# Kernel optimization log

Measured on AMD Instinct MI355X. Metric: run time of the kernel, lower is better.

Reference implementation:

```python
import jax, jax.numpy as jnp
import numpy as np
from math import factorial, sqrt

LMAX = 5
TAUS = [16, 16, 16, 16, 16, 16]
BATCH = 256


def _cg(j1, m1, j2, m2, j, m):
    """Standard (complex SO(3) basis) Clebsch-Gordan coefficient <j1 m1 j2 m2 | j m>."""
    if m1 + m2 != m or j < abs(j1 - j2) or j > j1 + j2:
        return 0.0
    f = factorial
    pref = sqrt((2 * j + 1) * f(j + j1 - j2) * f(j - j1 + j2) * f(j1 + j2 - j) / f(j1 + j2 + j + 1))
    pref *= sqrt(f(j + m) * f(j - m) * f(j1 - m1) * f(j1 + m1) * f(j2 - m2) * f(j2 + m2))
    kmin = max(0, j2 - j - m1, j1 + m2 - j)
    kmax = min(j1 + j2 - j, j1 - m1, j2 + m2)
    s = 0.0
    for k in range(kmin, kmax + 1):
        s += (-1) ** k / (f(k) * f(j1 + j2 - j - k) * f(j1 - m1 - k) * f(j2 + m2 - k)
                          * f(j - j2 + m1 + k) * f(j - j1 - m2 + k))
    return pref * s


def _pairs():
    # default CGNet ltuples: for each output l, all (l1, l2) with l1 <= l2 and triangle ineq.
    out = []
    for l in range(LMAX + 1):
        for l1 in range(LMAX + 1):
            for l2 in range(l1, LMAX + 1):
                if abs(l1 - l2) <= l <= l1 + l2:
                    out.append((l, l1, l2))
    return out


PAIRS = _pairs()  # 69 (l, l1, l2) tuples for lmax=5


def _cg_mat(l, l1, l2):
    M = np.zeros((2 * l1 + 1, 2 * l2 + 1, 2 * l + 1), dtype=np.float32)
    for m1 in range(-l1, l1 + 1):
        for m2 in range(-l2, l2 + 1):
            m = m1 + m2
            if -l <= m <= l:
                M[m1 + l1, m2 + l2, m + l] = _cg(l1, m1, l2, m2, l, m)
    return M


CG_MATS = {p: _cg_mat(*p) for p in PAIRS}
CUM_TAUS = np.concatenate([[0], (np.asarray(TAUS) * (2 * np.arange(LMAX + 1) + 1)).cumsum()]).astype(int)


def setup_inputs() -> dict:
    key = jax.random.key(0)
    Fs = jax.random.normal(key, (BATCH, int(CUM_TAUS[-1]), 2), dtype=jnp.float32)
    return {"Fs": Fs}


def reference(Fs) -> jnp.ndarray:
    """Sparse CG tensor product: for each (l,l1,l2) combine fragments F_l1, F_l2
    with CG coefficients into the l-output fragment; concat all fragments.
    Output: (B, cumu_tm_FF[-1], 2) with (m, tau) flattening per l fragment."""
    B = Fs.shape[0]
    frR, frI = [], []
    for l in range(LMAX + 1):
        seg = Fs[:, CUM_TAUS[l]:CUM_TAUS[l + 1]].reshape(B, 2 * l + 1, TAUS[l], 2)
        frR.append(seg[..., 0])
        frI.append(seg[..., 1])
    outs = [[] for _ in range(LMAX + 1)]
    for (l, l1, l2) in PAIRS:
        cg = jnp.asarray(CG_MATS[(l, l1, l2)])  # (2l1+1, 2l2+1, 2l+1)
        r1, i1, r2, i2 = frR[l1], frI[l1], frR[l2], frI[l2]
        e = lambda a, b: jnp.einsum('xym,bxi,byj->bmij', cg, a, b)
        oR = e(r1, r2) - e(i1, i2)           # complex multiply, real part
        oI = e(r1, i2) + e(i1, r2)           # imag part
        # (B, 2l+1, tau1*tau2, 2)
        outs[l].append(jnp.stack([oR, oI], axis=-1).reshape(B, 2 * l + 1, -1, 2))
    # per-l: concat channel blocks (t_offsets order), flatten (m, tau), concat over l
    return jnp.concatenate(
        [jnp.concatenate(outs[l], axis=2).reshape(B, -1, 2) for l in range(LMAX + 1)], axis=1)
```

## Files before the change

### kernel.cpp

```cpp
#include <hip/hip_runtime.h>
#include <vector>
#include <cmath>
#include <cstdint>


#define LMAXV 5
#define NTAU 16

static const int CUMT[7] = {0, 16, 64, 144, 256, 400, 576};

constexpr int F_ROWS   = 576;
constexpr int F4_ROWS  = 288;
constexpr int NBATCH   = 256;
constexpr int F4_PER_B = 457 * 128;
constexpr int BLK      = 256;
constexpr int NCHUNK   = 8;
constexpr int NCOEF    = 2211;
constexpr int MAXJC    = 58;

typedef float f32x4 __attribute__((ext_vector_type(4)));


static double factd(int n) { double r = 1.0; for (int i = 2; i <= n; ++i) r *= (double)i; return r; }

static double cg_coef(int j1, int m1, int j2, int m2, int j, int m) {
    if (m1 + m2 != m) return 0.0;
    double pref = std::sqrt((2.0 * j + 1.0) * factd(j + j1 - j2) * factd(j - j1 + j2) *
                            factd(j1 + j2 - j) / factd(j1 + j2 + j + 1));
    pref *= std::sqrt(factd(j + m) * factd(j - m) * factd(j1 - m1) * factd(j1 + m1) *
                      factd(j2 - m2) * factd(j2 + m2));
    int kmin = std::max(0, std::max(j2 - j - m1, j1 + m2 - j));
    int kmax = std::min(j1 + j2 - j, std::min(j1 - m1, j2 + m2));
    double s = 0.0;
    for (int k = kmin; k <= kmax; ++k) {
        s += ((k & 1) ? -1.0 : 1.0) /
             (factd(k) * factd(j1 + j2 - j - k) * factd(j1 - m1 - k) * factd(j2 + m2 - k) *
              factd(j - j2 + m1 + k) * factd(j - j1 - m2 + k));
    }
    return pref * s;
}

struct Tables { std::vector<int4> jobs; std::vector<float> coeffs; };

static const Tables& get_tables() {
    static Tables t = []() {
        Tables t;
        for (int l = 0; l <= LMAXV; ++l) {
            for (int m_idx = 0; m_idx < 2 * l + 1; ++m_idx) {
                int m = m_idx - l;
                for (int l1 = 0; l1 <= LMAXV; ++l1) {
                    for (int l2 = l1; l2 <= LMAXV; ++l2) {
                        if (!(std::abs(l1 - l2) <= l && l <= l1 + l2)) continue;
                        int lo = std::max(-l1, m - l2), hi = std::min(l1, m + l2);
                        int4 jb;
                        jb.x = (CUMT[l1] / 2 + (lo + l1) * 8) * 16;
                        jb.y = (CUMT[l2] / 2 + (m - lo + l2) * 8) * 16;
                        jb.z = hi - lo + 1;
                        jb.w = (int)t.coeffs.size();
                        for (int m1 = lo; m1 <= hi; ++m1)
                            t.coeffs.push_back((float)cg_coef(l1, m1, l2, m - m1, l, m));
                        t.jobs.push_back(jb);
                    }
                }
            }
        }
        return t;
    }();
    return t;
}


#define KBODY(N)                                                              \
    {                                                                         \
        f32x4 a[N], v[N]; float cc[N];                                        \
        _Pragma("unroll")                                                     \
        for (int k = 0; k < N; ++k) {                                         \
            a[k]  = *(const f32x4*)(sFb + ax + k * 128);                      \
            v[k]  = *(const f32x4*)(sFb + vy - k * 128);                      \
            cc[k] = sC[coff + k];                                             \
        }                                                                     \
        _Pragma("unroll")                                                     \
        for (int k = 0; k < N; ++k) {                                         \
            r00 = fmaf(cc[k], a[k].x * v[k].x - a[k].y * v[k].y, r00);        \
            i00 = fmaf(cc[k], a[k].x * v[k].y + a[k].y * v[k].x, i00);        \
            r01 = fmaf(cc[k], a[k].x * v[k].z - a[k].y * v[k].w, r01);        \
            i01 = fmaf(cc[k], a[k].x * v[k].w + a[k].y * v[k].z, i01);        \
            r10 = fmaf(cc[k], a[k].z * v[k].x - a[k].w * v[k].y, r10);        \
            i10 = fmaf(cc[k], a[k].z * v[k].y + a[k].w * v[k].x, i10);        \
            r11 = fmaf(cc[k], a[k].z * v[k].z - a[k].w * v[k].w, r11);        \
            i11 = fmaf(cc[k], a[k].z * v[k].w + a[k].w * v[k].z, i11);        \
        }                                                                     \
    }

__global__ __launch_bounds__(256) void cg_tp_kernel(
    const f32x4* __restrict__ Fs, f32x4* __restrict__ out,
    const int4* __restrict__ jobs, const float* __restrict__ coeffs)
{
    __shared__ f32x4 sF[F4_ROWS];
    __shared__ float sC[NCOEF];
    __shared__ int4  sJ[MAXJC];

    const int tid   = threadIdx.x;
    const int batch = blockIdx.x >> 3;
    const int chunk = blockIdx.x & (NCHUNK - 1);
    const int jbase = chunk * 57;
    const int jcnt  = (chunk == NCHUNK - 1) ? 58 : 57;

    {
        const f32x4* __restrict__ Fb4 = Fs + (size_t)batch * F4_ROWS;
        for (int t = tid; t < F4_ROWS; t += BLK) sF[t] = Fb4[t];
        for (int t = tid; t < NCOEF;   t += BLK) sC[t] = coeffs[t];
        for (int t = tid; t < jcnt;    t += BLK) sJ[t] = jobs[jbase + t];
    }
    __syncthreads();

    const int wv   = tid >> 6;
    const int lane = tid & 63;
    const int ip   = lane >> 3;
    const int jp   = lane & 7;
    const char* __restrict__ sFb = (const char*)sF;

    f32x4* __restrict__ outb =
        out + (size_t)batch * F4_PER_B + (size_t)jbase * 128;

    for (int jj = wv; jj < jcnt; jj += 4) {
        const int4 jbv = sJ[jj];
        const int ax   = __builtin_amdgcn_readfirstlane(jbv.x) + ip * 16;
        const int vy   = __builtin_amdgcn_readfirstlane(jbv.y) + jp * 16;
        const int cnt  = __builtin_amdgcn_readfirstlane(jbv.z);
        const int coff = __builtin_amdgcn_readfirstlane(jbv.w);

        float r00 = 0.f, i00 = 0.f, r01 = 0.f, i01 = 0.f;
        float r10 = 0.f, i10 = 0.f, r11 = 0.f, i11 = 0.f;

        switch (cnt) {
            case 1:  KBODY(1)  break;
            case 2:  KBODY(2)  break;
            case 3:  KBODY(3)  break;
            case 4:  KBODY(4)  break;
            case 5:  KBODY(5)  break;
            case 6:  KBODY(6)  break;
            case 7:  KBODY(7)  break;
            case 8:  KBODY(8)  break;
            case 9:  KBODY(9)  break;
            case 10: KBODY(10) break;
            default: KBODY(11) break;
        }

        f32x4 s0; s0.x = r00; s0.y = i00; s0.z = r01; s0.w = i01;
        f32x4 s1; s1.x = r10; s1.y = i10; s1.z = r11; s1.w = i11;
        f32x4* __restrict__ po = outb + (size_t)jj * 128 + ip * 16 + jp;
        po[0] = s0;
        po[8] = s1;
    }
}


extern "C" void kernel_launch(void* const* d_in, const int* in_sizes, int n_in,
                              void* d_out, int out_size, void* d_ws, size_t ws_size,
                              hipStream_t stream) {
    const Tables& t = get_tables();

    char*  ws       = (char*)d_ws;
    int4*  d_jobs   = (int4*)ws;
    size_t jbytes   = t.jobs.size() * sizeof(int4);
    size_t coff     = (jbytes + 255) & ~(size_t)255;
    float* d_coeffs = (float*)(ws + coff);

    hipMemcpyAsync(d_jobs, t.jobs.data(), jbytes, hipMemcpyHostToDevice, stream);
    hipMemcpyAsync(d_coeffs, t.coeffs.data(), t.coeffs.size() * sizeof(float),
                   hipMemcpyHostToDevice, stream);

    const f32x4* Fs  = (const f32x4*)d_in[0];
    f32x4*       out = (f32x4*)d_out;

    cg_tp_kernel<<<NBATCH * NCHUNK, BLK, 0, stream>>>(Fs, out, d_jobs, d_coeffs);
}
```

Before: 57.57 us.

## Make blocks persistent over batches with work-balanced job groups and double-buffered inputs

Blocks now iterate over 32 batches each instead of one. The 457 jobs are split into 128 groups balanced by coefficient count, and each block loads the coefficient and job tables once into LDS. The next batch's fragment is prefetched into registers while the current batch is computed, then written to the other LDS buffer. This amortises the table loads and balances work across blocks, at the cost of fewer blocks (1024), a barrier per phase, and more LDS per block.

```diff
diff --git a/kernel.cpp b/kernel.cpp
--- a/kernel.cpp
+++ b/kernel.cpp
@@ -9,14 +9,15 @@
 
 static const int CUMT[7] = {0, 16, 64, 144, 256, 400, 576};
 
-constexpr int F_ROWS   = 576;
 constexpr int F4_ROWS  = 288;
+constexpr int FBYTES   = F4_ROWS * 16;
 constexpr int NBATCH   = 256;
 constexpr int F4_PER_B = 457 * 128;
 constexpr int BLK      = 256;
-constexpr int NCHUNK   = 8;
+constexpr int NJOBS    = 457;
 constexpr int NCOEF    = 2211;
-constexpr int MAXJC    = 58;
+constexpr int NGRP     = 128;
+constexpr int NPHASE   = 32;
 
 typedef float f32x4 __attribute__((ext_vector_type(4)));
 
@@ -40,7 +41,7 @@
     return pref * s;
 }
 
-struct Tables { std::vector<int4> jobs; std::vector<float> coeffs; };
+struct Tables { std::vector<int4> jobs; std::vector<float> coeffs; std::vector<uint16_t> grp; };
 
 static const Tables& get_tables() {
     static Tables t = []() {
@@ -64,6 +65,15 @@
                 }
             }
         }
+        t.grp.assign(NGRP + 1, 0);
+        int total = 0; for (auto& j : t.jobs) total += j.z;
+        int jpos = 0; long cum = 0;
+        for (int g = 0; g < NGRP; ++g) {
+            t.grp[g] = (uint16_t)jpos;
+            long target = ((long)total * (g + 1) + NGRP / 2) / NGRP;
+            while (jpos < NJOBS && cum < target) { cum += t.jobs[jpos].z; ++jpos; }
+        }
+        t.grp[NGRP] = (uint16_t)NJOBS;
         return t;
     }();
     return t;
@@ -92,66 +102,84 @@
         }                                                                     \
     }
 
-__global__ __launch_bounds__(256) void cg_tp_kernel(
+__global__ __launch_bounds__(256, 4) void cg_tp_kernel(
     const f32x4* __restrict__ Fs, f32x4* __restrict__ out,
-    const int4* __restrict__ jobs, const float* __restrict__ coeffs)
+    const int4* __restrict__ jobs, const float* __restrict__ coeffs,
+    const uint16_t* __restrict__ grp)
 {
-    __shared__ f32x4 sF[F4_ROWS];
+    __shared__ f32x4 sF[2][F4_ROWS];
     __shared__ float sC[NCOEF];
-    __shared__ int4  sJ[MAXJC];
+    __shared__ int4  sJ[NJOBS];
 
     const int tid   = threadIdx.x;
-    const int batch = blockIdx.x >> 3;
-    const int chunk = blockIdx.x & (NCHUNK - 1);
-    const int jbase = chunk * 57;
-    const int jcnt  = (chunk == NCHUNK - 1) ? 58 : 57;
-
+    const int gid   = blockIdx.x & (NGRP - 1);
+    const int blane = blockIdx.x >> 7;
+
+    for (int t = tid; t < NCOEF; t += BLK) sC[t] = coeffs[t];
+    for (int t = tid; t < NJOBS; t += BLK) sJ[t] = jobs[t];
     {
-        const f32x4* __restrict__ Fb4 = Fs + (size_t)batch * F4_ROWS;
-        for (int t = tid; t < F4_ROWS; t += BLK) sF[t] = Fb4[t];
-        for (int t = tid; t < NCOEF;   t += BLK) sC[t] = coeffs[t];
-        for (int t = tid; t < jcnt;    t += BLK) sJ[t] = jobs[jbase + t];
+        const f32x4* __restrict__ F0 = Fs + (size_t)blane * F4_ROWS;
+        sF[0][tid] = F0[tid];
+        if (tid < F4_ROWS - BLK) sF[0][BLK + tid] = F0[BLK + tid];
     }
     __syncthreads();
+
+    const int js = grp[gid], je = grp[gid + 1];
 
     const int wv   = tid >> 6;
     const int lane = tid & 63;
     const int ip   = lane >> 3;
     const int jp   = lane & 7;
-    const char* __restrict__ sFb = (const char*)sF;
-
-    f32x4* __restrict__ outb =
-        out + (size_t)batch * F4_PER_B + (size_t)jbase * 128;
-
-    for (int jj = wv; jj < jcnt; jj += 4) {
-        const int4 jbv = sJ[jj];
-        const int ax   = __builtin_amdgcn_readfirstlane(jbv.x) + ip * 16;
-        const int vy   = __builtin_amdgcn_readfirstlane(jbv.y) + jp * 16;
-        const int cnt  = __builtin_amdgcn_readfirstlane(jbv.z);
-        const int coff = __builtin_amdgcn_readfirstlane(jbv.w);
-
-        float r00 = 0.f, i00 = 0.f, r01 = 0.f, i01 = 0.f;
-        float r10 = 0.f, i10 = 0.f, r11 = 0.f, i11 = 0.f;
-
-        switch (cnt) {
-            case 1:  KBODY(1)  break;
-            case 2:  KBODY(2)  break;
-            case 3:  KBODY(3)  break;
-            case 4:  KBODY(4)  break;
-            case 5:  KBODY(5)  break;
-            case 6:  KBODY(6)  break;
-            case 7:  KBODY(7)  break;
-            case 8:  KBODY(8)  break;
-            case 9:  KBODY(9)  break;
-            case 10: KBODY(10) break;
-            default: KBODY(11) break;
-        }
-
-        f32x4 s0; s0.x = r00; s0.y = i00; s0.z = r01; s0.w = i01;
-        f32x4 s1; s1.x = r10; s1.y = i10; s1.z = r11; s1.w = i11;
-        f32x4* __restrict__ po = outb + (size_t)jj * 128 + ip * 16 + jp;
-        po[0] = s0;
-        po[8] = s1;
+
+    for (int p = 0; p < NPHASE; ++p) {
+        const int batch = p * 8 + blane;
+
+        f32x4 r0, r1;
+        if (p < NPHASE - 1) {
+            const f32x4* __restrict__ Fn = Fs + (size_t)(batch + 8) * F4_ROWS;
+            r0 = Fn[tid];
+            if (tid < F4_ROWS - BLK) r1 = Fn[BLK + tid];
+        }
+
+        const char* __restrict__ sFb = (const char*)&sF[p & 1][0];
+        f32x4* __restrict__ outb = out + (size_t)batch * F4_PER_B;
+
+        for (int jj = js + wv; jj < je; jj += 4) {
+            const int4 jbv = sJ[jj];
+            const int ax   = __builtin_amdgcn_readfirstlane(jbv.x) + ip * 16;
+            const int vy   = __builtin_amdgcn_readfirstlane(jbv.y) + jp * 16;
+            const int cnt  = __builtin_amdgcn_readfirstlane(jbv.z);
+            const int coff = __builtin_amdgcn_readfirstlane(jbv.w);
+
+            float r00 = 0.f, i00 = 0.f, r01 = 0.f, i01 = 0.f;
+            float r10 = 0.f, i10 = 0.f, r11 = 0.f, i11 = 0.f;
+
+            switch (cnt) {
+                case 1:  KBODY(1)  break;
+                case 2:  KBODY(2)  break;
+                case 3:  KBODY(3)  break;
+                case 4:  KBODY(4)  break;
+                case 5:  KBODY(5)  break;
+                case 6:  KBODY(6)  break;
+                case 7:  KBODY(7)  break;
+                case 8:  KBODY(8)  break;
+                case 9:  KBODY(9)  break;
+                case 10: KBODY(10) break;
+                default: KBODY(11) break;
+            }
+
+            f32x4 s0; s0.x = r00; s0.y = i00; s0.z = r01; s0.w = i01;
+            f32x4 s1; s1.x = r10; s1.y = i10; s1.z = r11; s1.w = i11;
+            f32x4* __restrict__ po = outb + (size_t)jj * 128 + ip * 16 + jp;
+            po[0] = s0;
+            po[8] = s1;
+        }
+
+        if (p < NPHASE - 1) {
+            sF[(p + 1) & 1][tid] = r0;
+            if (tid < F4_ROWS - BLK) sF[(p + 1) & 1][BLK + tid] = r1;
+        }
+        __syncthreads();
     }
 }
 
@@ -161,18 +189,22 @@
                               hipStream_t stream) {
     const Tables& t = get_tables();
 
-    char*  ws       = (char*)d_ws;
-    int4*  d_jobs   = (int4*)ws;
-    size_t jbytes   = t.jobs.size() * sizeof(int4);
-    size_t coff     = (jbytes + 255) & ~(size_t)255;
-    float* d_coeffs = (float*)(ws + coff);
-
-    hipMemcpyAsync(d_jobs, t.jobs.data(), jbytes, hipMemcpyHostToDevice, stream);
+    char*     ws       = (char*)d_ws;
+    int4*     d_jobs   = (int4*)ws;
+    size_t    coff     = (NJOBS * sizeof(int4) + 255) & ~(size_t)255;
+    float*    d_coeffs = (float*)(ws + coff);
+    size_t    goff     = (coff + NCOEF * sizeof(float) + 255) & ~(size_t)255;
+    uint16_t* d_grp    = (uint16_t*)(ws + goff);
+
+    hipMemcpyAsync(d_jobs, t.jobs.data(), t.jobs.size() * sizeof(int4),
+                   hipMemcpyHostToDevice, stream);
     hipMemcpyAsync(d_coeffs, t.coeffs.data(), t.coeffs.size() * sizeof(float),
                    hipMemcpyHostToDevice, stream);
+    hipMemcpyAsync(d_grp, t.grp.data(), t.grp.size() * sizeof(uint16_t),
+                   hipMemcpyHostToDevice, stream);
 
     const f32x4* Fs  = (const f32x4*)d_in[0];
     f32x4*       out = (f32x4*)d_out;
 
-    cg_tp_kernel<<<NBATCH * NCHUNK, BLK, 0, stream>>>(Fs, out, d_jobs, d_coeffs);
-}
+    cg_tp_kernel<<<NGRP * 8, BLK, 0, stream>>>(Fs, out, d_jobs, d_coeffs, d_grp);
+}
```

Result: slower. 86.48 us (+50.2%).

## Split work per batch into two cost-balanced halves with 512-thread blocks

Applied to the files above, without the earlier changes.

Replaces eight fixed job chunks of 256 threads per batch with two 512-thread blocks per batch, split at the point where the cumulative coefficient count reaches half. This cuts the redundant loading of inputs and the coefficient table into shared memory from eight times to twice per batch, and balances the work between the two blocks. The per-count switch over fully unrolled bodies is replaced by a loop unrolled by four plus a small remainder switch, which shrinks code size but may lengthen dependency chains. Fewer, larger blocks (512 total) may leave some compute units underused.

```diff
diff --git a/kernel.cpp b/kernel.cpp
--- a/kernel.cpp
+++ b/kernel.cpp
@@ -9,14 +9,12 @@
 
 static const int CUMT[7] = {0, 16, 64, 144, 256, 400, 576};
 
-constexpr int F_ROWS   = 576;
 constexpr int F4_ROWS  = 288;
 constexpr int NBATCH   = 256;
 constexpr int F4_PER_B = 457 * 128;
-constexpr int BLK      = 256;
-constexpr int NCHUNK   = 8;
+constexpr int BLK      = 512;
+constexpr int NJOBS    = 457;
 constexpr int NCOEF    = 2211;
-constexpr int MAXJC    = 58;
 
 typedef float f32x4 __attribute__((ext_vector_type(4)));
 
@@ -40,7 +38,7 @@
     return pref * s;
 }
 
-struct Tables { std::vector<int4> jobs; std::vector<float> coeffs; };
+struct Tables { std::vector<int4> jobs; std::vector<float> coeffs; int split; };
 
 static const Tables& get_tables() {
     static Tables t = []() {
@@ -64,20 +62,24 @@
                 }
             }
         }
+        int total = 0; for (auto& j : t.jobs) total += j.z;
+        int cum = 0, s = 0;
+        for (int j = 0; j < NJOBS; ++j) { cum += t.jobs[j].z; if (cum * 2 >= total) { s = j + 1; break; } }
+        t.split = s;
         return t;
     }();
     return t;
 }
 
 
-#define KBODY(N)                                                              \
+#define QBODY(N)                                                              \
     {                                                                         \
         f32x4 a[N], v[N]; float cc[N];                                        \
         _Pragma("unroll")                                                     \
         for (int k = 0; k < N; ++k) {                                         \
-            a[k]  = *(const f32x4*)(sFb + ax + k * 128);                      \
-            v[k]  = *(const f32x4*)(sFb + vy - k * 128);                      \
-            cc[k] = sC[coff + k];                                             \
+            a[k]  = *(const f32x4*)(sFb + axq + k * 128);                     \
+            v[k]  = *(const f32x4*)(sFb + vyq - k * 128);                     \
+            cc[k] = sC[coq + k];                                              \
         }                                                                     \
         _Pragma("unroll")                                                     \
         for (int k = 0; k < N; ++k) {                                         \
@@ -92,27 +94,29 @@
         }                                                                     \
     }
 
-__global__ __launch_bounds__(256) void cg_tp_kernel(
+__global__ __launch_bounds__(512, 4) void cg_tp_kernel(
     const f32x4* __restrict__ Fs, f32x4* __restrict__ out,
-    const int4* __restrict__ jobs, const float* __restrict__ coeffs)
+    const int4* __restrict__ jobs, const float* __restrict__ coeffs,
+    int split)
 {
     __shared__ f32x4 sF[F4_ROWS];
     __shared__ float sC[NCOEF];
-    __shared__ int4  sJ[MAXJC];
+    __shared__ int4  sJ[NJOBS];
 
     const int tid   = threadIdx.x;
-    const int batch = blockIdx.x >> 3;
-    const int chunk = blockIdx.x & (NCHUNK - 1);
-    const int jbase = chunk * 57;
-    const int jcnt  = (chunk == NCHUNK - 1) ? 58 : 57;
+    const int batch = blockIdx.x >> 1;
+    const int chunk = blockIdx.x & 1;
 
     {
         const f32x4* __restrict__ Fb4 = Fs + (size_t)batch * F4_ROWS;
-        for (int t = tid; t < F4_ROWS; t += BLK) sF[t] = Fb4[t];
-        for (int t = tid; t < NCOEF;   t += BLK) sC[t] = coeffs[t];
-        for (int t = tid; t < jcnt;    t += BLK) sJ[t] = jobs[jbase + t];
+        if (tid < F4_ROWS) sF[tid] = Fb4[tid];
+        for (int t = tid; t < NCOEF; t += BLK) sC[t] = coeffs[t];
+        for (int t = tid; t < NJOBS; t += BLK) sJ[t] = jobs[t];
     }
     __syncthreads();
+
+    const int js = chunk ? split : 0;
+    const int je = chunk ? NJOBS : split;
 
     const int wv   = tid >> 6;
     const int lane = tid & 63;
@@ -120,10 +124,9 @@
     const int jp   = lane & 7;
     const char* __restrict__ sFb = (const char*)sF;
 
-    f32x4* __restrict__ outb =
-        out + (size_t)batch * F4_PER_B + (size_t)jbase * 128;
+    f32x4* __restrict__ outb = out + (size_t)batch * F4_PER_B;
 
-    for (int jj = wv; jj < jcnt; jj += 4) {
+    for (int jj = js + wv; jj < je; jj += 8) {
         const int4 jbv = sJ[jj];
         const int ax   = __builtin_amdgcn_readfirstlane(jbv.x) + ip * 16;
         const int vy   = __builtin_amdgcn_readfirstlane(jbv.y) + jp * 16;
@@ -133,18 +136,19 @@
         float r00 = 0.f, i00 = 0.f, r01 = 0.f, i01 = 0.f;
         float r10 = 0.f, i10 = 0.f, r11 = 0.f, i11 = 0.f;
 
-        switch (cnt) {
-            case 1:  KBODY(1)  break;
-            case 2:  KBODY(2)  break;
-            case 3:  KBODY(3)  break;
-            case 4:  KBODY(4)  break;
-            case 5:  KBODY(5)  break;
-            case 6:  KBODY(6)  break;
-            case 7:  KBODY(7)  break;
-            case 8:  KBODY(8)  break;
-            case 9:  KBODY(9)  break;
-            case 10: KBODY(10) break;
-            default: KBODY(11) break;
+        int k0 = 0;
+        for (; k0 + 4 <= cnt; k0 += 4) {
+            const int axq = ax + k0 * 128, vyq = vy - k0 * 128, coq = coff + k0;
+            QBODY(4)
+        }
+        {
+            const int axq = ax + k0 * 128, vyq = vy - k0 * 128, coq = coff + k0;
+            switch (cnt - k0) {
+                case 1: QBODY(1) break;
+                case 2: QBODY(2) break;
+                case 3: QBODY(3) break;
+                default: break;
+            }
         }
 
         f32x4 s0; s0.x = r00; s0.y = i00; s0.z = r01; s0.w = i01;
@@ -163,7 +167,7 @@
 
     char*  ws       = (char*)d_ws;
     int4*  d_jobs   = (int4*)ws;
-    size_t jbytes   = t.jobs.size() * sizeof(int4);
+    size_t jbytes   = NJOBS * sizeof(int4);
     size_t coff     = (jbytes + 255) & ~(size_t)255;
     float* d_coeffs = (float*)(ws + coff);
 
@@ -174,5 +178,5 @@
     const f32x4* Fs  = (const f32x4*)d_in[0];
     f32x4*       out = (f32x4*)d_out;
 
-    cg_tp_kernel<<<NBATCH * NCHUNK, BLK, 0, stream>>>(Fs, out, d_jobs, d_coeffs);
+    cg_tp_kernel<<<NBATCH * 2, BLK, 0, stream>>>(Fs, out, d_jobs, d_coeffs, t.split);
 }
```

Result: slower. 66.56 us (+15.6%).
